# Kernel tuning notes

Measured on AMD Instinct MI355X. Metric: run time of the kernel, lower is better.

## Reference

```python
import jax, jax.numpy as jnp
import numpy as np

H, B, F, D1, D21, D22, C = 10, 16384, 4, 2048, 2048, 2048, 2
OBS_X, OBS_Y, RADIUS = 40.0, 15.0, 6.0


def setup_inputs() -> dict:
    key = jax.random.key(0)
    ks = jax.random.split(key, 12)
    s = 0.02  # weight scale
    return {
        'x':   jax.random.normal(ks[0], (B, F), jnp.float32),
        'W1':  jax.random.normal(ks[1], (H, F, D1), jnp.float32) * s,
        'b1':  jnp.zeros((H, D1), jnp.float32),
        'W21': jax.random.normal(ks[2], (H, D1, D21), jnp.float32) * s,
        'b21': jnp.zeros((H, D21), jnp.float32),
        'W22': jax.random.normal(ks[3], (H, D1, D22), jnp.float32) * s,
        'b22': jnp.zeros((H, D22), jnp.float32),
        'W31': jax.random.normal(ks[4], (H, D21, C), jnp.float32) * s,
        'b31': jnp.zeros((H, C), jnp.float32),
        'W32': jax.random.normal(ks[5], (H, D22, C), jnp.float32) * s,
        'b32': jnp.zeros((H, C), jnp.float32),
        'wt':  jnp.ones((H,), jnp.float32),
        'mean': jax.random.normal(ks[6], (F,), jnp.float32),
        'std':  jnp.ones((F,), jnp.float32),
        'sgn': 1,
        'itr': 0,
    }


def reference(x, W1, b1, W21, b21, W22, b22, W31, b31, W32, b32, wt, mean, std, sgn, itr):
    # x: [B,F]; un-normalized state x0 = x*std + mean
    x0 = x * std + mean

    # --- 10-head small-MLP ensemble (batched over heads via einsum) ---
    h1  = jax.nn.relu(jnp.einsum('bf,hfd->hbd', x, W1) + b1[:, None, :])      # [H,B,D1]
    x21 = jax.nn.relu(jnp.einsum('hbd,hde->hbe', h1, W21) + b21[:, None, :])  # [H,B,D21]
    x22 = jax.nn.relu(jnp.einsum('hbd,hde->hbe', h1, W22) + b22[:, None, :])  # [H,B,D22]
    x31 = jnp.einsum('hbe,hec->hbc', x21, W31) + b31[:, None, :]              # [H,B,C] nominal control
    x32 = 4.0 * jax.nn.sigmoid(jnp.einsum('hbe,hec->hbc', x22, W32) + b32[:, None, :])  # [H,B,C] CBF params

    # --- dCBF constraint (shared across heads; depends only on x0) ---
    px, py, theta, v = x0[:, 0], x0[:, 1], x0[:, 2], x0[:, 3]
    dx, dy = px - OBS_X, py - OBS_Y
    st, ct = jnp.sin(theta), jnp.cos(theta)
    barrier = dx * dx + dy * dy - RADIUS * RADIUS                 # [B]
    barrier_dot = 2.0 * dx * v * ct + 2.0 * dy * v * st          # [B]
    Lf2b = 2.0 * v * v                                            # [B]
    LgLfbu1 = -2.0 * dx * v * st + 2.0 * dy * v * ct
    LgLfbu2 = 2.0 * dx * ct + 2.0 * dy * st
    G = jnp.stack([-LgLfbu1, -LgLfbu2], axis=-1)                  # [B,C]

    # sgn == 1 -> same branch for every head (i==0 or sgn==1)
    h_rhs = Lf2b + (x32[..., 0] + x32[..., 1]) * barrier_dot + x32[..., 0] * x32[..., 1] * barrier  # [H,B]

    # --- batched QP: min 0.5 u'u - x31'u  s.t. G u <= h  (Q = I) ---
    # closed-form single-constraint active set: u = x31 - relu(G.x31 - h)/||G||^2 * G
    Gu = jnp.einsum('bc,hbc->hb', G, x31)                         # [H,B]
    GG = jnp.sum(G * G, axis=-1)                                  # [B]
    lam = jax.nn.relu(Gu - h_rhs) / GG                            # [H,B]
    u = x31 - lam[..., None] * G[None, :, :]                      # [H,B,C]

    # --- softmax-weighted ensemble sum ---
    w = jax.nn.softmax(wt)                                        # [H]
    return jnp.einsum('h,hbc->bc', w, u)                          # [B,C]
```

## Files before the change

### kernel.cpp

```cpp
#include <hip/hip_runtime.h>
#include <hip/hip_bf16.h>
#include <stdint.h>

#define H_  10
#define B_  16384
#define F_  4
#define D_  2048
#define C_  2

typedef __attribute__((ext_vector_type(8)))  short  short8;
typedef __attribute__((ext_vector_type(16))) float  floatx16;

typedef const uint32_t __attribute__((address_space(1))) gu32;
typedef uint32_t       __attribute__((address_space(3))) lu32;

__device__ __forceinline__ void async16(const void* g, void* l) {
    __builtin_amdgcn_global_load_lds((gu32*)g, (lu32*)l, 16, 0, 0);
}

__device__ __forceinline__ short8 bc8(uint4 v) { return __builtin_bit_cast(short8, v); }

__device__ __forceinline__ uint32_t packbf(float a, float b) {
    a = fmaxf(a, 0.f); b = fmaxf(b, 0.f);
    const uint32_t ax = __builtin_bit_cast(uint32_t, a) + 0x8000u;
    const uint32_t bx = __builtin_bit_cast(uint32_t, b) + 0x8000u;
    return (ax >> 16) | (bx & 0xFFFF0000u);
}

__device__ __forceinline__ uint32_t f2bf(float f) {
    union { float f; uint32_t u; } a; a.f = f;
    uint32_t u = a.u;
    u += 0x7FFF + ((u >> 16) & 1);
    return u >> 16;
}
__device__ __forceinline__ uint32_t pack2bf(float a, float b) {
    return f2bf(a) | (f2bf(b) << 16);
}


__global__ __launch_bounds__(256) void k_convert(
    const float* __restrict__ W21, const float* __restrict__ W22,
    uint16_t* __restrict__ Bc)
{
    __shared__ float tile[64][65];
    const int z = blockIdx.z;
    const int h = z % H_;
    const float* src = (z < H_ ? W21 : W22) + (size_t)h * D_ * D_;
    uint16_t*   dst  = Bc + (size_t)h * 2 * D_ * D_ + (z < H_ ? 0 : (size_t)D_ * D_);
    const int k0 = blockIdx.x * 64, n0 = blockIdx.y * 64;
    const int t = threadIdx.x;

    const int c4 = (t & 15) * 4;
    const int rb = (t >> 4) * 4;
#pragma unroll
    for (int i = 0; i < 4; i++) {
        const float4 v = *(const float4*)(src + (size_t)(k0 + rb + i) * D_ + n0 + c4);
        tile[rb + i][c4 + 0] = v.x; tile[rb + i][c4 + 1] = v.y;
        tile[rb + i][c4 + 2] = v.z; tile[rb + i][c4 + 3] = v.w;
    }
    __syncthreads();
    const int n = t >> 2;
    const int cb = (t & 3) * 2;
#pragma unroll
    for (int j = 0; j < 2; j++) {
        const int kk = (cb + j) * 8;
        uint32_t pk[4];
#pragma unroll
        for (int e = 0; e < 4; e++)
            pk[e] = pack2bf(tile[kk + 2 * e][n], tile[kk + 2 * e + 1][n]);
        *(uint4*)(dst + (size_t)(n0 + n) * D_ + k0 + kk) = make_uint4(pk[0], pk[1], pk[2], pk[3]);
    }
}

__global__ __launch_bounds__(256) void k_zero(uint4* p, int n4) {
    const int i = blockIdx.x * 256 + threadIdx.x;
    if (i < n4) p[i] = make_uint4(0u, 0u, 0u, 0u);
}

__global__ __launch_bounds__(256) void k_h1(
    const float* __restrict__ x, const float* __restrict__ W1,
    const float* __restrict__ b1, uint16_t* __restrict__ h1t, int h)
{
    const int t = threadIdx.x;
    const int kc = t & 127;
    const int rh = t >> 7;
    const int k0 = kc * 16;
    const float* W1h = W1 + (size_t)h * F_ * D_;
    float w[4][16], bb[16];
#pragma unroll
    for (int f = 0; f < 4; f++)
#pragma unroll
        for (int j = 0; j < 16; j += 4) {
            const float4 v = *(const float4*)(W1h + f * D_ + k0 + j);
            w[f][j] = v.x; w[f][j+1] = v.y; w[f][j+2] = v.z; w[f][j+3] = v.w;
        }
#pragma unroll
    for (int j = 0; j < 16; j += 4) {
        const float4 v = *(const float4*)(b1 + (size_t)h * D_ + k0 + j);
        bb[j] = v.x; bb[j+1] = v.y; bb[j+2] = v.z; bb[j+3] = v.w;
    }
    const int rowBase = blockIdx.x * 16 + rh * 8;
#pragma unroll
    for (int rr = 0; rr < 8; rr++) {
        const int row = rowBase + rr;
        const float4 xv = *(const float4*)(x + (size_t)row * 4);
        uint32_t pk[8];
#pragma unroll
        for (int j = 0; j < 16; j += 2) {
            float aa = fmaf(xv.x, w[0][j], bb[j]);
            aa = fmaf(xv.y, w[1][j], aa);
            aa = fmaf(xv.z, w[2][j], aa);
            aa = fmaf(xv.w, w[3][j], aa);
            float bv = fmaf(xv.x, w[0][j+1], bb[j+1]);
            bv = fmaf(xv.y, w[1][j+1], bv);
            bv = fmaf(xv.z, w[2][j+1], bv);
            bv = fmaf(xv.w, w[3][j+1], bv);
            pk[j >> 1] = packbf(aa, bv);
        }
        uint16_t* d = h1t + (size_t)row * D_ + k0;
        *(uint4*)d       = make_uint4(pk[0], pk[1], pk[2], pk[3]);
        *(uint4*)(d + 8) = make_uint4(pk[4], pk[5], pk[6], pk[7]);
    }
}

__global__ __launch_bounds__(256, 2) void k_gemm(
    const uint16_t* __restrict__ h1t, const uint16_t* __restrict__ Bcw,
    const float* __restrict__ b21, const float* __restrict__ b22,
    const float* __restrict__ W31, const float* __restrict__ W32,
    float* __restrict__ acc31, float* __restrict__ acc32, int h)
{
    __shared__ uint4 smem[3072];

    const int bid = blockIdx.x;
    const int xcd = bid & 7, idx = bid >> 3;
    const int mt = xcd * 16 + (idx & 15), nt = idx >> 4;
    const int mBase = mt * 128, nBase = nt * 256;

    const int t = threadIdx.x;
    const int lane = t & 63, wid = t >> 6;
    const int l31 = lane & 31, hi = lane >> 5;

    const uint16_t* Abase = h1t + (size_t)mBase * D_;
    const uint16_t* Bbase = Bcw + (size_t)h * (4096 * (size_t)D_) + (size_t)nBase * D_;
    int aoff[2], boff[4];
#pragma unroll
    for (int j = 0; j < 2; j++) {
        const int unit = j * 256 + t;
        const int rp = unit >> 3, uu = (unit & 7) ^ (rp & 7);
        aoff[j] = (rp * 2 + (uu & 1)) * D_ + (uu >> 1) * 8;
    }
#pragma unroll
    for (int j = 0; j < 4; j++) {
        const int unit = j * 256 + t;
        const int rp = unit >> 3, uu = (unit & 7) ^ (rp & 7);
        boff[j] = (rp * 2 + (uu & 1)) * D_ + (uu >> 1) * 8;
    }
    const int wbase = wid * 64;

    auto stageTile = [&](int buf, int kt) {
#pragma unroll
        for (int j = 0; j < 2; j++)
            async16(Abase + aoff[j] + kt, smem + buf * 512 + j * 256 + wbase);
#pragma unroll
        for (int j = 0; j < 4; j++)
            async16(Bbase + boff[j] + kt, smem + 1024 + buf * 1024 + j * 256 + wbase);
    };

    const int rpl = l31 >> 1;
    const int par = l31 & 1;
    const int x7p = rpl & 7;

    floatx16 acc[4][2];
#pragma unroll
    for (int mi = 0; mi < 4; mi++)
#pragma unroll
        for (int nj = 0; nj < 2; nj++)
#pragma unroll
            for (int e = 0; e < 16; e++) acc[mi][nj][e] = 0.f;

    stageTile(0, 0);
    stageTile(1, 32);

    for (int tt = 0; tt < 64; ++tt) {
        if (tt == 63) { asm volatile("s_waitcnt vmcnt(0)" ::: "memory"); }
        else          { asm volatile("s_waitcnt vmcnt(6)" ::: "memory"); }
        __builtin_amdgcn_sched_barrier(0);
        __builtin_amdgcn_s_barrier();

        const int ab = (tt & 1) * 512;
        const int bb = 1024 + (tt & 1) * 1024;

        __builtin_amdgcn_s_setprio(1);
#pragma unroll
        for (int kk = 0; kk < 2; kk++) {
            const int u = ((((kk * 2 + hi) << 1) | par) ^ x7p);
            short8 af[4], bf[2];
#pragma unroll
            for (int mi = 0; mi < 4; mi++)
                af[mi] = bc8(smem[ab + (mi * 16 + rpl) * 8 + u]);
#pragma unroll
            for (int nj = 0; nj < 2; nj++)
                bf[nj] = bc8(smem[bb + (wid * 32 + nj * 16 + rpl) * 8 + u]);
#pragma unroll
            for (int mi = 0; mi < 4; mi++)
#pragma unroll
                for (int nj = 0; nj < 2; nj++)
                    acc[mi][nj] = __builtin_amdgcn_mfma_f32_32x32x16_bf16(
                        af[mi], bf[nj], acc[mi][nj], 0, 0, 0);
        }
        __builtin_amdgcn_s_setprio(0);

        __builtin_amdgcn_s_barrier();
        __builtin_amdgcn_sched_barrier(0);
        if (tt < 62) stageTile(tt & 1, (tt + 2) * 32);
    }

    const int p    = nBase >> 11;
    const int nloc = nBase & 2047;
    const float* b2p = (p ? b22 : b21) + (size_t)h * D_;
    const float* W3p = (p ? W32 : W31) + (size_t)h * D_ * C_;
    float* ab2 = (p ? acc32 : acc31) + (size_t)h * B_ * C_;

    float bs[2], w3x[2], w3y[2];
#pragma unroll
    for (int nj = 0; nj < 2; nj++) {
        const int e = nloc + wid * 64 + nj * 32 + l31;
        bs[nj] = b2p[e];
        const float2 w2 = *(const float2*)(W3p + e * 2);
        w3x[nj] = w2.x; w3y[nj] = w2.y;
    }
#pragma unroll
    for (int mi = 0; mi < 4; mi++)
#pragma unroll
        for (int r = 0; r < 16; r++) {
            const float v0 = fmaxf(acc[mi][0][r] + bs[0], 0.f);
            const float v1 = fmaxf(acc[mi][1][r] + bs[1], 0.f);
            float s0 = fmaf(v0, w3x[0], v1 * w3x[1]);
            float s1 = fmaf(v0, w3y[0], v1 * w3y[1]);
#pragma unroll
            for (int off = 1; off < 32; off <<= 1) {
                s0 += __shfl_xor(s0, off, 64);
                s1 += __shfl_xor(s1, off, 64);
            }
            if (l31 == 0) {
                const int row = mBase + mi * 32 + (r & 3) + 8 * (r >> 2) + 4 * hi;
                atomicAdd(&ab2[row * C_ + 0], s0);
                atomicAdd(&ab2[row * C_ + 1], s1);
            }
        }
}

__global__ __launch_bounds__(256) void k_final(
    const float* __restrict__ x,
    const float* __restrict__ acc31, const float* __restrict__ acc32,
    const float* __restrict__ b31, const float* __restrict__ b32,
    const float* __restrict__ wt, const float* __restrict__ mean,
    const float* __restrict__ stdv, float* __restrict__ out)
{
    const int b = blockIdx.x * 256 + threadIdx.x;
    const float4 xb = *(const float4*)(x + (size_t)b * 4);
    const float px = xb.x * stdv[0] + mean[0];
    const float py = xb.y * stdv[1] + mean[1];
    const float th = xb.z * stdv[2] + mean[2];
    const float v  = xb.w * stdv[3] + mean[3];
    const float dx = px - 40.0f, dy = py - 15.0f;
    const float st = sinf(th), ct = cosf(th);
    const float barrier = dx * dx + dy * dy - 36.0f;
    const float bdot = 2.f * dx * v * ct + 2.f * dy * v * st;
    const float Lf2b = 2.f * v * v;
    const float G0 = -(-2.f * dx * v * st + 2.f * dy * v * ct);
    const float G1 = -(2.f * dx * ct + 2.f * dy * st);
    const float GG = G0 * G0 + G1 * G1;

    float we[H_];
    float wmax = wt[0];
    for (int h = 1; h < H_; h++) wmax = fmaxf(wmax, wt[h]);
    float wsum = 0.f;
    for (int h = 0; h < H_; h++) { we[h] = expf(wt[h] - wmax); wsum += we[h]; }

    float o0 = 0.f, o1 = 0.f;
#pragma unroll
    for (int h = 0; h < H_; h++) {
        const size_t idx = ((size_t)h * B_ + b) * 2;
        const float x310 = acc31[idx]     + b31[h * 2];
        const float x311 = acc31[idx + 1] + b31[h * 2 + 1];
        const float z0 = acc32[idx]     + b32[h * 2];
        const float z1 = acc32[idx + 1] + b32[h * 2 + 1];
        const float x320 = 4.f / (1.f + expf(-z0));
        const float x321 = 4.f / (1.f + expf(-z1));
        const float hr = Lf2b + (x320 + x321) * bdot + x320 * x321 * barrier;
        const float Gu = G0 * x310 + G1 * x311;
        const float lam = fmaxf(Gu - hr, 0.f) / GG;
        o0 += we[h] * (x310 - lam * G0);
        o1 += we[h] * (x311 - lam * G1);
    }
    out[b * 2]     = o0 / wsum;
    out[b * 2 + 1] = o1 / wsum;
}

extern "C" void kernel_launch(void* const* d_in, const int* in_sizes, int n_in,
                              void* d_out, int out_size, void* d_ws, size_t ws_size,
                              hipStream_t stream)
{
    const float* x    = (const float*)d_in[0];
    const float* W1   = (const float*)d_in[1];
    const float* b1   = (const float*)d_in[2];
    const float* W21  = (const float*)d_in[3];
    const float* b21  = (const float*)d_in[4];
    const float* W22  = (const float*)d_in[5];
    const float* b22  = (const float*)d_in[6];
    const float* W31  = (const float*)d_in[7];
    const float* b31  = (const float*)d_in[8];
    const float* W32  = (const float*)d_in[9];
    const float* b32  = (const float*)d_in[10];
    const float* wt   = (const float*)d_in[11];
    const float* mean = (const float*)d_in[12];
    const float* stdv = (const float*)d_in[13];
    float* out = (float*)d_out;

    char* ws = (char*)d_ws;
    uint16_t* Bc   = (uint16_t*)(ws);
    float* acc31   = (float*)(ws + 167772160);
    float* acc32   = (float*)(ws + 169082880);
    uint16_t* h1t  = (uint16_t*)(ws + 170393600);

    k_convert<<<dim3(32, 32, 20), 256, 0, stream>>>(W21, W22, Bc);
    k_zero<<<dim3(640), 256, 0, stream>>>((uint4*)acc31, 163840);
    for (int h = 0; h < H_; ++h) {
        k_h1<<<dim3(1024), 256, 0, stream>>>(x, W1, b1, h1t, h);
        k_gemm<<<dim3(2048), 256, 0, stream>>>(h1t, Bc, b21, b22, W31, W32,
                                               acc31, acc32, h);
    }
    k_final<<<dim3(64), 256, 0, stream>>>(x, acc31, acc32, b31, b32, wt, mean, stdv, out);
}
```

Baseline: 3.682 ms.

## Load B operand directly to registers in MFMA-fragment layout, stage only A in LDS

The weight transpose kernel now writes B in a pre-swizzled layout that matches the MFMA 32x32x16 fragment order. The GEMM then loads B fragments straight from global memory into registers, prefetching one step ahead. Only the A tile goes through LDS, and the K step per stage doubles to 64 with a new XOR swizzle. This is meant to cut LDS traffic and LDS capacity use for B, at the cost of more VGPRs, direct global loads whose latency must be hidden, and redundant loads of B across waves and blocks.

New measurement: 3.400 ms. -7.6%, faster.

```diff
diff --git a/kernel.cpp b/kernel.cpp
--- a/kernel.cpp
+++ b/kernel.cpp
@@ -68,7 +68,10 @@
 #pragma unroll
         for (int e = 0; e < 4; e++)
             pk[e] = pack2bf(tile[kk + 2 * e][n], tile[kk + 2 * e + 1][n]);
-        *(uint4*)(dst + (size_t)(n0 + n) * D_ + k0 + kk) = make_uint4(pk[0], pk[1], pk[2], pk[3]);
+        const int N = n0 + n, K = k0 + kk;
+        const size_t off = (size_t)(N >> 5) * 65536 + (size_t)(K >> 4) * 512
+                         + (size_t)((K >> 3) & 1) * 256 + (size_t)(N & 31) * 8;
+        *(uint4*)(dst + off) = make_uint4(pk[0], pk[1], pk[2], pk[3]);
     }
 }
 
@@ -129,7 +132,7 @@
     const float* __restrict__ W31, const float* __restrict__ W32,
     float* __restrict__ acc31, float* __restrict__ acc32, int h)
 {
-    __shared__ uint4 smem[3072];
+    __shared__ uint4 smemA[2048];
 
     const int bid = blockIdx.x;
     const int xcd = bid & 7, idx = bid >> 3;
@@ -141,34 +144,29 @@
     const int l31 = lane & 31, hi = lane >> 5;
 
     const uint16_t* Abase = h1t + (size_t)mBase * D_;
-    const uint16_t* Bbase = Bcw + (size_t)h * (4096 * (size_t)D_) + (size_t)nBase * D_;
-    int aoff[2], boff[4];
-#pragma unroll
-    for (int j = 0; j < 2; j++) {
-        const int unit = j * 256 + t;
-        const int rp = unit >> 3, uu = (unit & 7) ^ (rp & 7);
-        aoff[j] = (rp * 2 + (uu & 1)) * D_ + (uu >> 1) * 8;
-    }
+    int aoff[4];
 #pragma unroll
     for (int j = 0; j < 4; j++) {
         const int unit = j * 256 + t;
-        const int rp = unit >> 3, uu = (unit & 7) ^ (rp & 7);
-        boff[j] = (rp * 2 + (uu & 1)) * D_ + (uu >> 1) * 8;
+        const int row = unit >> 3;
+        const int cc = (unit & 7) ^ (row & 7) ^ ((row >> 3) & 3);
+        aoff[j] = row * D_ + cc * 8;
     }
     const int wbase = wid * 64;
 
-    auto stageTile = [&](int buf, int kt) {
-#pragma unroll
-        for (int j = 0; j < 2; j++)
-            async16(Abase + aoff[j] + kt, smem + buf * 512 + j * 256 + wbase);
+    auto stageA = [&](int buf, int kt) {
 #pragma unroll
         for (int j = 0; j < 4; j++)
-            async16(Bbase + boff[j] + kt, smem + 1024 + buf * 1024 + j * 256 + wbase);
+            async16(Abase + aoff[j] + kt, smemA + buf * 1024 + j * 256 + wbase);
     };
 
-    const int rpl = l31 >> 1;
-    const int par = l31 & 1;
-    const int x7p = rpl & 7;
+    const uint16_t* Bhead = Bcw + (size_t)h * (4096 * (size_t)D_);
+    const uint16_t* bptr[2];
+#pragma unroll
+    for (int nj = 0; nj < 2; nj++) {
+        const int nf = (nBase >> 5) + wid * 2 + nj;
+        bptr[nj] = Bhead + (size_t)nf * 65536 + (size_t)hi * 256 + (size_t)l31 * 8;
+    }
 
     floatx16 acc[4][2];
 #pragma unroll
@@ -178,41 +176,54 @@
 #pragma unroll
             for (int e = 0; e < 16; e++) acc[mi][nj][e] = 0.f;
 
-    stageTile(0, 0);
-    stageTile(1, 32);
-
-    for (int tt = 0; tt < 64; ++tt) {
-        if (tt == 63) { asm volatile("s_waitcnt vmcnt(0)" ::: "memory"); }
-        else          { asm volatile("s_waitcnt vmcnt(6)" ::: "memory"); }
+    uint4 bA[2][4], bB[2][4];
+    const int x7 = l31 & 7, s3 = l31 >> 3;
+
+    auto halfiter = [&](int tt, uint4 (&bcur)[2][4], uint4 (&bnxt)[2][4]) {
+        asm volatile("s_waitcnt vmcnt(12)" ::: "memory");
         __builtin_amdgcn_sched_barrier(0);
         __builtin_amdgcn_s_barrier();
-
-        const int ab = (tt & 1) * 512;
-        const int bb = 1024 + (tt & 1) * 1024;
-
+        const int tn = (tt < 31) ? tt + 1 : 31;
+#pragma unroll
+        for (int nj = 0; nj < 2; nj++)
+#pragma unroll
+            for (int kk = 0; kk < 4; kk++)
+                bnxt[nj][kk] = *(const uint4*)(bptr[nj] + (size_t)(tn * 4 + kk) * 512);
+        const int buf = tt & 1;
         __builtin_amdgcn_s_setprio(1);
 #pragma unroll
-        for (int kk = 0; kk < 2; kk++) {
-            const int u = ((((kk * 2 + hi) << 1) | par) ^ x7p);
-            short8 af[4], bf[2];
+        for (int kk = 0; kk < 4; kk++) {
+            const int u7 = (kk * 2 + hi) ^ x7 ^ s3;
+            short8 af[4];
 #pragma unroll
             for (int mi = 0; mi < 4; mi++)
-                af[mi] = bc8(smem[ab + (mi * 16 + rpl) * 8 + u]);
-#pragma unroll
-            for (int nj = 0; nj < 2; nj++)
-                bf[nj] = bc8(smem[bb + (wid * 32 + nj * 16 + rpl) * 8 + u]);
+                af[mi] = bc8(smemA[buf * 1024 + (mi * 32 + l31) * 8 + u7]);
 #pragma unroll
             for (int mi = 0; mi < 4; mi++)
 #pragma unroll
                 for (int nj = 0; nj < 2; nj++)
                     acc[mi][nj] = __builtin_amdgcn_mfma_f32_32x32x16_bf16(
-                        af[mi], bf[nj], acc[mi][nj], 0, 0, 0);
+                        af[mi], bc8(bcur[nj][kk]), acc[mi][nj], 0, 0, 0);
         }
         __builtin_amdgcn_s_setprio(0);
-
         __builtin_amdgcn_s_barrier();
         __builtin_amdgcn_sched_barrier(0);
-        if (tt < 62) stageTile(tt & 1, (tt + 2) * 32);
+        stageA(buf, ((tt < 30) ? tt + 2 : 31) * 64);
+    };
+
+    stageA(0, 0);
+    stageA(1, 64);
+    __builtin_amdgcn_sched_barrier(0);
+#pragma unroll
+    for (int nj = 0; nj < 2; nj++)
+#pragma unroll
+        for (int kk = 0; kk < 4; kk++)
+            bA[nj][kk] = *(const uint4*)(bptr[nj] + (size_t)kk * 512);
+
+#pragma unroll 1
+    for (int it = 0; it < 16; ++it) {
+        halfiter(2 * it,     bA, bB);
+        halfiter(2 * it + 1, bB, bA);
     }
 
     const int p    = nBase >> 11;
```

## Enlarge GEMM tile to 256x256 with K=64 stages and 128KB dynamic LDS

Applied to the files above, without the earlier changes.

The second-layer GEMM block tile grows from 128x256 to 256x256 and the K step from 32 to 64. This doubles the per-wave accumulators to 8x2 MFMA tiles and raises arithmetic intensity per LDS load. The LDS layout switches to a row-major swizzle, the double-buffered staging uses 128KB of dynamic shared memory, and the K loop is unrolled by two buffers. In exchange, occupancy drops to one block per CU, there is more register pressure (256 accumulator floats per thread), and the grid is halved to 1024 blocks.

New measurement: 9.149 ms. 2.48x slower.

```diff
diff --git a/kernel.cpp b/kernel.cpp
--- a/kernel.cpp
+++ b/kernel.cpp
@@ -123,18 +123,18 @@
     }
 }
 
-__global__ __launch_bounds__(256, 2) void k_gemm(
+__global__ __launch_bounds__(256, 1) void k_gemm(
     const uint16_t* __restrict__ h1t, const uint16_t* __restrict__ Bcw,
     const float* __restrict__ b21, const float* __restrict__ b22,
     const float* __restrict__ W31, const float* __restrict__ W32,
     float* __restrict__ acc31, float* __restrict__ acc32, int h)
 {
-    __shared__ uint4 smem[3072];
+    extern __shared__ uint4 smem[];
 
     const int bid = blockIdx.x;
     const int xcd = bid & 7, idx = bid >> 3;
-    const int mt = xcd * 16 + (idx & 15), nt = idx >> 4;
-    const int mBase = mt * 128, nBase = nt * 256;
+    const int mt = xcd * 8 + (idx & 7), nt = idx >> 3;
+    const int mBase = mt * 256, nBase = nt * 256;
 
     const int t = threadIdx.x;
     const int lane = t & 63, wid = t >> 6;
@@ -142,77 +142,69 @@
 
     const uint16_t* Abase = h1t + (size_t)mBase * D_;
     const uint16_t* Bbase = Bcw + (size_t)h * (4096 * (size_t)D_) + (size_t)nBase * D_;
-    int aoff[2], boff[4];
-#pragma unroll
-    for (int j = 0; j < 2; j++) {
+    int soff[8];
+#pragma unroll
+    for (int j = 0; j < 8; j++) {
         const int unit = j * 256 + t;
-        const int rp = unit >> 3, uu = (unit & 7) ^ (rp & 7);
-        aoff[j] = (rp * 2 + (uu & 1)) * D_ + (uu >> 1) * 8;
-    }
-#pragma unroll
-    for (int j = 0; j < 4; j++) {
-        const int unit = j * 256 + t;
-        const int rp = unit >> 3, uu = (unit & 7) ^ (rp & 7);
-        boff[j] = (rp * 2 + (uu & 1)) * D_ + (uu >> 1) * 8;
+        const int row = unit >> 3;
+        const int cc = (unit & 7) ^ (row & 7) ^ ((row >> 3) & 3);
+        soff[j] = row * D_ + cc * 8;
     }
     const int wbase = wid * 64;
 
     auto stageTile = [&](int buf, int kt) {
 #pragma unroll
-        for (int j = 0; j < 2; j++)
-            async16(Abase + aoff[j] + kt, smem + buf * 512 + j * 256 + wbase);
-#pragma unroll
-        for (int j = 0; j < 4; j++)
-            async16(Bbase + boff[j] + kt, smem + 1024 + buf * 1024 + j * 256 + wbase);
+        for (int j = 0; j < 8; j++)
+            async16(Abase + soff[j] + kt, smem + buf * 2048 + j * 256 + wbase);
+#pragma unroll
+        for (int j = 0; j < 8; j++)
+            async16(Bbase + soff[j] + kt, smem + 4096 + buf * 2048 + j * 256 + wbase);
     };
 
-    const int rpl = l31 >> 1;
-    const int par = l31 & 1;
-    const int x7p = rpl & 7;
-
-    floatx16 acc[4][2];
-#pragma unroll
-    for (int mi = 0; mi < 4; mi++)
+    floatx16 acc[8][2];
+#pragma unroll
+    for (int mi = 0; mi < 8; mi++)
 #pragma unroll
         for (int nj = 0; nj < 2; nj++)
 #pragma unroll
             for (int e = 0; e < 16; e++) acc[mi][nj][e] = 0.f;
 
-    stageTile(0, 0);
-    stageTile(1, 32);
-
-    for (int tt = 0; tt < 64; ++tt) {
-        if (tt == 63) { asm volatile("s_waitcnt vmcnt(0)" ::: "memory"); }
-        else          { asm volatile("s_waitcnt vmcnt(6)" ::: "memory"); }
+    const int x7 = l31 & 7, s3 = l31 >> 3;
+
+    auto kIter = [&](int tt, int buf) {
+        asm volatile("s_waitcnt vmcnt(16)" ::: "memory");
         __builtin_amdgcn_sched_barrier(0);
         __builtin_amdgcn_s_barrier();
-
-        const int ab = (tt & 1) * 512;
-        const int bb = 1024 + (tt & 1) * 1024;
-
-        __builtin_amdgcn_s_setprio(1);
-#pragma unroll
-        for (int kk = 0; kk < 2; kk++) {
-            const int u = ((((kk * 2 + hi) << 1) | par) ^ x7p);
-            short8 af[4], bf[2];
-#pragma unroll
-            for (int mi = 0; mi < 4; mi++)
-                af[mi] = bc8(smem[ab + (mi * 16 + rpl) * 8 + u]);
+        const uint4* Ab = smem + buf * 2048;
+        const uint4* Bb = smem + 4096 + buf * 2048;
+#pragma unroll
+        for (int kk = 0; kk < 4; kk++) {
+            const int u7 = (kk * 2 + hi) ^ x7 ^ s3;
+            short8 bf[2];
 #pragma unroll
             for (int nj = 0; nj < 2; nj++)
-                bf[nj] = bc8(smem[bb + (wid * 32 + nj * 16 + rpl) * 8 + u]);
-#pragma unroll
-            for (int mi = 0; mi < 4; mi++)
+                bf[nj] = bc8(Bb[(wbase + nj * 32 + l31) * 8 + u7]);
+#pragma unroll
+            for (int mi = 0; mi < 8; mi++) {
+                const short8 af = bc8(Ab[(mi * 32 + l31) * 8 + u7]);
 #pragma unroll
                 for (int nj = 0; nj < 2; nj++)
                     acc[mi][nj] = __builtin_amdgcn_mfma_f32_32x32x16_bf16(
-                        af[mi], bf[nj], acc[mi][nj], 0, 0, 0);
+                        af, bf[nj], acc[mi][nj], 0, 0, 0);
+            }
         }
-        __builtin_amdgcn_s_setprio(0);
-
         __builtin_amdgcn_s_barrier();
         __builtin_amdgcn_sched_barrier(0);
-        if (tt < 62) stageTile(tt & 1, (tt + 2) * 32);
+        stageTile(buf, ((tt < 30) ? tt + 2 : 31) * 64);
+    };
+
+    stageTile(0, 0);
+    stageTile(1, 64);
+
+#pragma unroll 1
+    for (int it = 0; it < 16; ++it) {
+        kIter(2 * it,     0);
+        kIter(2 * it + 1, 1);
     }
 
     const int p    = nBase >> 11;
@@ -230,7 +222,7 @@
         w3x[nj] = w2.x; w3y[nj] = w2.y;
     }
 #pragma unroll
-    for (int mi = 0; mi < 4; mi++)
+    for (int mi = 0; mi < 8; mi++)
 #pragma unroll
         for (int r = 0; r < 16; r++) {
             const float v0 = fmaxf(acc[mi][0][r] + bs[0], 0.f);
@@ -324,12 +316,19 @@
     float* acc32   = (float*)(ws + 169082880);
     uint16_t* h1t  = (uint16_t*)(ws + 170393600);
 
+    static bool attr_done = false;
+    if (!attr_done) {
+        hipFuncSetAttribute(reinterpret_cast<const void*>(k_gemm),
+                            hipFuncAttributeMaxDynamicSharedMemorySize, 131072);
+        attr_done = true;
+    }
+
     k_convert<<<dim3(32, 32, 20), 256, 0, stream>>>(W21, W22, Bc);
     k_zero<<<dim3(640), 256, 0, stream>>>((uint4*)acc31, 163840);
     for (int h = 0; h < H_; ++h) {
         k_h1<<<dim3(1024), 256, 0, stream>>>(x, W1, b1, h1t, h);
-        k_gemm<<<dim3(2048), 256, 0, stream>>>(h1t, Bc, b21, b22, W31, W32,
-                                               acc31, acc32, h);
+        k_gemm<<<dim3(1024), 256, 131072, stream>>>(h1t, Bc, b21, b22, W31, W32,
+                                                    acc31, acc32, h);
     }
     k_final<<<dim3(64), 256, 0, stream>>>(x, acc31, acc32, b31, b32, wt, mean, stdv, out);
 }
```
